# Kernel tuning notes

Hardware: AMD Instinct MI355X
Metric: run time of the kernel (lower is better)

Reference implementation:

```python
import jax, jax.numpy as jnp
import numpy as np
import math

NUM_HEADS = 16


def _alibi_slopes(num_heads: int):
    # geometric sequence for power-of-2 head counts (paper's scheme)
    def slopes_pow2(n):
        start = 2.0 ** (-(2.0 ** (-(math.log2(n) - 3))))
        return [start * (start ** i) for i in range(n)]
    if math.log2(num_heads).is_integer():
        return slopes_pow2(num_heads)
    c = 2 ** math.floor(math.log2(num_heads))
    extra = slopes_pow2(2 * c)[0::2][: num_heads - c]
    return slopes_pow2(c) + extra


def setup_inputs() -> dict:
    key = jax.random.key(0)
    kq, kk, kv = jax.random.split(key, 3)
    B, H, S, D = 2, NUM_HEADS, 2048, 64
    q = jax.random.normal(kq, (B, H, S, D), dtype=jnp.float32)
    k = jax.random.normal(kk, (B, H, S, D), dtype=jnp.float32)
    v = jax.random.normal(kv, (B, H, S, D), dtype=jnp.float32)
    return {"q": q, "k": k, "v": v}


def reference(q, k, v):
    B, H, Sq, D = q.shape
    Sk = k.shape[2]
    slopes = jnp.asarray(_alibi_slopes(H), dtype=jnp.float32)  # [H]
    pos = jnp.arange(Sk)
    # abs relative positions (symmetric, non-causal) as in the source
    rel = jnp.abs(pos[None, :] - pos[:, None]).astype(jnp.float32)  # [Sk, Sk]
    alibi = -slopes[:, None, None] * rel[None, :Sq, :]  # [H, Sq, Sk]
    scores = jnp.einsum("bhqd,bhkd->bhqk", q, k) / math.sqrt(D)
    scores = scores + alibi[None]
    probs = jax.nn.softmax(scores, axis=-1)
    return jnp.einsum("bhqk,bhkd->bhqd", probs, v)
```

## Files before the change

kernel.cpp:

```cpp
#include <hip/hip_runtime.h>
#include <hip/hip_bf16.h>
#include <math.h>

typedef __bf16 bf16;
typedef __attribute__((ext_vector_type(8))) bf16 bf16x8;
typedef __attribute__((ext_vector_type(2))) bf16 bf16x2;
typedef __attribute__((ext_vector_type(16))) float f32x16;
typedef __attribute__((ext_vector_type(4))) unsigned int uint4v;

#define SQ 2048
#define DH 64
#define NH 16
#define QBLK 64
#define KVT 64
#define NKVT (SQ / KVT)
#define LOG2E 1.44269504088896340736f

#define PBUF  16384
#define LDSV  8192
#define LDS_BYTES 32768

__device__ __forceinline__ int swz(int row, int colbyte) {
    return row * 128 + (colbyte ^ ((row & 7) << 4));
}

__device__ __forceinline__ float fast_exp2(float x) {
#if __has_builtin(__builtin_amdgcn_exp2f)
    return __builtin_amdgcn_exp2f(x);
#else
    return exp2f(x);
#endif
}

__device__ __forceinline__ unsigned pkbf16(float a, float b) {
    union { bf16x2 h; unsigned u; } x;
    x.h = (bf16x2){(bf16)a, (bf16)b};
    return x.u;
}

#if __has_builtin(__builtin_amdgcn_permlane32_swap)
__device__ __forceinline__ void plswap(unsigned &a, unsigned &b) {
    typedef __attribute__((ext_vector_type(2))) unsigned int uint2v;
    uint2v r = __builtin_amdgcn_permlane32_swap(a, b, false, false);
    a = r[0]; b = r[1];
}
#else
__device__ __forceinline__ void plswap(unsigned &a, unsigned &b) {
    asm volatile("v_permlane32_swap_b32 %0, %1" : "+v"(a), "+v"(b));
}
#endif

#if __has_builtin(__builtin_amdgcn_global_load_lds)
#define HAVE_GLL 1
__device__ __forceinline__ void async_copy16(const bf16* g, char* l) {
    __builtin_amdgcn_global_load_lds(
        (const __attribute__((address_space(1))) unsigned int*)g,
        (__attribute__((address_space(3))) unsigned int*)l, 16, 0, 0);
}
#else
#define HAVE_GLL 0
#endif

union FragU { uint4v u; bf16x8 b; };

__global__ __launch_bounds__(256)
void alibi_prep_kernel(const float* __restrict__ K, const float* __restrict__ V,
                       bf16* __restrict__ Kb, bf16* __restrict__ Vtb) {
    __shared__ bf16 lt[64][72];
    const int t  = threadIdx.x;
    const int s0 = blockIdx.x * 64;
    const int bh = blockIdx.y;
    if (blockIdx.z == 0) {
        const float* src = K + (size_t)bh * SQ * DH + (size_t)s0 * DH;
        bf16* dst = Kb + (size_t)bh * SQ * DH + (size_t)s0 * DH;
#pragma unroll
        for (int i = 0; i < 2; ++i) {
            int idx = t + 256 * i;
            int row = idx >> 3, c8 = idx & 7;
            const float* p = src + row * DH + c8 * 8;
            float4 a = *(const float4*)p, b = *(const float4*)(p + 4);
            bf16x8 pk = {(bf16)a.x,(bf16)a.y,(bf16)a.z,(bf16)a.w,
                         (bf16)b.x,(bf16)b.y,(bf16)b.z,(bf16)b.w};
            *(bf16x8*)(dst + row * DH + c8 * 8) = pk;
        }
    } else {
        const float* src = V + (size_t)bh * SQ * DH + (size_t)s0 * DH;
#pragma unroll
        for (int i = 0; i < 2; ++i) {
            int idx = t + 256 * i;
            int row = idx >> 3, c8 = idx & 7;
            const float* p = src + row * DH + c8 * 8;
            float4 a = *(const float4*)p, b = *(const float4*)(p + 4);
            bf16 e[8] = {(bf16)a.x,(bf16)a.y,(bf16)a.z,(bf16)a.w,
                         (bf16)b.x,(bf16)b.y,(bf16)b.z,(bf16)b.w};
#pragma unroll
            for (int j = 0; j < 8; ++j) lt[c8 * 8 + j][row] = e[j];
        }
        __syncthreads();
        bf16* dst = Vtb + (size_t)bh * DH * SQ;
#pragma unroll
        for (int i = 0; i < 2; ++i) {
            int idx = t + 256 * i;
            int d = idx >> 3, c8 = idx & 7;
            *(bf16x8*)(dst + (size_t)d * SQ + s0 + c8 * 8) = *(const bf16x8*)&lt[d][c8 * 8];
        }
    }
}

__global__ __launch_bounds__(256, 4)
void alibi_attn_kernel(const float* __restrict__ Q, const bf16* __restrict__ Kb,
                       const bf16* __restrict__ Vtb, float* __restrict__ Out) {
    __shared__ __align__(16) char lds[LDS_BYTES];
    const int tid   = threadIdx.x;
    const int lane  = tid & 63;
    const int wave  = tid >> 6;
    const int par   = wave >> 1;
    const int kind  = wave & 1;
    const int qhalf = wave & 1;
    const int r32   = lane & 31;
    const int hi    = lane >> 5;
    const int l8    = lane >> 3;

    const int b  = blockIdx.x;
    const int qd = b >> 8, i = b & 255;
    int r;
    if      (qd == 0) r = i;
    else if (qd == 1) r = 511 - i;
    else if (qd == 2) r = 512 + i;
    else              r = 1023 - i;
    const int h   = 15 - (r >> 6);
    const int sub = r & 63;
    const int bh  = (sub >> 5) * NH + h;
    const int q0  = (sub & 31) * QBLK;

    const float slope2  = exp2f(-0.5f * (float)(h + 1)) * LOG2E;
    const float SLOPE2N = -slope2;
    const float QSCALE  = 0.125f * LOG2E;

    const int D = (int)(24.0f / slope2);
    const int a0 = q0 - D;
    const int tmin = (a0 <= 0) ? 0 : (a0 >> 6);
    const int tmax = min(NKVT - 1, (q0 + QBLK - 1 + D) >> 6);
    const int nsteps = ((tmax - tmin + 1) + 1) >> 1;

    const size_t base = (size_t)bh * SQ * DH;
    const float* Qp = Q + base;
    const bf16*  Kp = Kb + base;
    const bf16*  Vp = Vtb + base;
    float*       Op = Out + base;

    const int qrow = q0 + qhalf * 32 + r32;
    bf16x8 qfrag[4];
#pragma unroll
    for (int dstep = 0; dstep < 4; ++dstep) {
        const float* sq = Qp + (size_t)qrow * DH + dstep * 16 + hi * 8;
        float4 a = *(const float4*)sq, bb = *(const float4*)(sq + 4);
        qfrag[dstep] = (bf16x8){(bf16)(a.x*QSCALE),(bf16)(a.y*QSCALE),
                                (bf16)(a.z*QSCALE),(bf16)(a.w*QSCALE),
                                (bf16)(bb.x*QSCALE),(bf16)(bb.y*QSCALE),
                                (bf16)(bb.z*QSCALE),(bf16)(bb.w*QSCALE)};
    }

    f32x16 oacc[2];
#pragma unroll
    for (int d = 0; d < 2; ++d)
#pragma unroll
        for (int rr = 0; rr < 16; ++rr) oacc[d][rr] = 0.f;
    float ps0 = 0.f, ps1 = 0.f, ps2 = 0.f, ps3 = 0.f;
    const float qh = (float)(qrow - 4 * hi);

    const int cswz = ((lane & 7) << 4) ^ (l8 << 4);
    char* const sbuf = lds + par * PBUF + kind * LDSV;
    const char* const cbuf = lds + par * PBUF;

    for (int s = 0; s < nsteps; ++s) {
        const int tc = tmin + 2 * s + par;
        const int ts = min(tc, tmax);

        {
            const int kv0s = ts * KVT;
            if (kind == 0) {
#pragma unroll
                for (int c = 0; c < 8; ++c) {
                    const int row = c * 8 + l8;
                    const bf16* gK = Kp + (size_t)(kv0s + row) * DH + (cswz >> 1);
#if HAVE_GLL
                    async_copy16(gK, sbuf + c * 1024);
#else
                    *(bf16x8*)(sbuf + c * 1024 + lane * 16) = *(const bf16x8*)gK;
#endif
                }
            } else {
#pragma unroll
                for (int c = 0; c < 8; ++c) {
                    const int row = c * 8 + l8;
                    const bf16* gV = Vp + (size_t)row * SQ + kv0s + (cswz >> 1);
#if HAVE_GLL
                    async_copy16(gV, sbuf + c * 1024);
#else
                    *(bf16x8*)(sbuf + c * 1024 + lane * 16) = *(const bf16x8*)gV;
#endif
                }
            }
        }
        asm volatile("s_waitcnt vmcnt(0)" ::: "memory");
        __builtin_amdgcn_s_barrier();
        __builtin_amdgcn_sched_barrier(0);

        if (tc <= tmax) {
            const int kv0 = tc * KVT;

            f32x16 sacc[2];
            __builtin_amdgcn_s_setprio(1);
#pragma unroll
            for (int blk = 0; blk < 2; ++blk) {
                f32x16 acc;
#pragma unroll
                for (int rr = 0; rr < 16; ++rr) acc[rr] = 0.f;
#pragma unroll
                for (int dstep = 0; dstep < 4; ++dstep) {
                    bf16x8 kf = *(const bf16x8*)(cbuf + swz(blk * 32 + r32, dstep * 32 + hi * 16));
                    acc = __builtin_amdgcn_mfma_f32_32x32x16_bf16(kf, qfrag[dstep], acc, 0, 0, 0);
                }
                sacc[blk] = acc;
            }
            __builtin_amdgcn_s_setprio(0);

            const float gq = qh - (float)kv0;
            float p[32];
#pragma unroll
            for (int blk = 0; blk < 2; ++blk)
#pragma unroll
                for (int reg = 0; reg < 16; ++reg) {
                    const int krel = (reg & 3) + 8 * (reg >> 2) + 32 * blk;
                    float d = gq - (float)krel;
                    float s2 = fmaf(SLOPE2N, fabsf(d), sacc[blk][reg]);
                    float e = fast_exp2(s2);
                    p[blk * 16 + reg] = e;
                    if ((reg & 3) == 0) ps0 += e;
                    else if ((reg & 3) == 1) ps1 += e;
                    else if ((reg & 3) == 2) ps2 += e;
                    else ps3 += e;
                }

            __builtin_amdgcn_s_setprio(1);
#pragma unroll
            for (int kstep = 0; kstep < 4; ++kstep) {
                const int b16 = (kstep >> 1) * 16;
                const int R = (kstep & 1) * 8;
                unsigned w0 = pkbf16(p[b16 + R + 0], p[b16 + R + 1]);
                unsigned w1 = pkbf16(p[b16 + R + 2], p[b16 + R + 3]);
                unsigned w2 = pkbf16(p[b16 + R + 4], p[b16 + R + 5]);
                unsigned w3 = pkbf16(p[b16 + R + 6], p[b16 + R + 7]);
                plswap(w0, w2);
                plswap(w1, w3);
                FragU pf; pf.u = (uint4v){w0, w1, w2, w3};
#pragma unroll
                for (int dblk = 0; dblk < 2; ++dblk) {
                    bf16x8 vf = *(const bf16x8*)(cbuf + LDSV + swz(dblk * 32 + r32, kstep * 32 + hi * 16));
                    oacc[dblk] = __builtin_amdgcn_mfma_f32_32x32x16_bf16(vf, pf.b, oacc[dblk], 0, 0, 0);
                }
            }
            __builtin_amdgcn_s_setprio(0);
        }
        __builtin_amdgcn_s_barrier();
        __builtin_amdgcn_sched_barrier(0);
    }

    float psum = (ps0 + ps1) + (ps2 + ps3);
    psum += __shfl_xor(psum, 32);

    __syncthreads();
    float* ep = (float*)lds + qhalf * (64 * 36);
    float* slot = ep + lane * 36;
    if (par == 1) {
#pragma unroll
        for (int dblk = 0; dblk < 2; ++dblk)
#pragma unroll
            for (int g2 = 0; g2 < 4; ++g2)
                *(float4*)(slot + dblk * 16 + g2 * 4) =
                    (float4){oacc[dblk][4*g2+0], oacc[dblk][4*g2+1],
                             oacc[dblk][4*g2+2], oacc[dblk][4*g2+3]};
        slot[32] = psum;
    }
    __syncthreads();
    if (par == 0) {
#pragma unroll
        for (int dblk = 0; dblk < 2; ++dblk)
#pragma unroll
            for (int g2 = 0; g2 < 4; ++g2) {
                float4 o = *(const float4*)(slot + dblk * 16 + g2 * 4);
                oacc[dblk][4*g2+0] += o.x; oacc[dblk][4*g2+1] += o.y;
                oacc[dblk][4*g2+2] += o.z; oacc[dblk][4*g2+3] += o.w;
            }
        psum += slot[32];

        const float inv = 1.f / psum;
#pragma unroll
        for (int dblk = 0; dblk < 2; ++dblk)
#pragma unroll
            for (int g2 = 0; g2 < 4; ++g2) {
                float4 o = {oacc[dblk][4*g2+0] * inv, oacc[dblk][4*g2+1] * inv,
                            oacc[dblk][4*g2+2] * inv, oacc[dblk][4*g2+3] * inv};
                *(float4*)(Op + (size_t)qrow * DH + dblk * 32 + g2 * 8 + hi * 4) = o;
            }
    }
}

extern "C" void kernel_launch(void* const* d_in, const int* in_sizes, int n_in,
                              void* d_out, int out_size, void* d_ws, size_t ws_size,
                              hipStream_t stream) {
    const float* q = (const float*)d_in[0];
    const float* k = (const float*)d_in[1];
    const float* v = (const float*)d_in[2];
    float* out = (float*)d_out;
    const int BH = in_sizes[0] / (SQ * DH);
    bf16* Kb  = (bf16*)d_ws;
    bf16* Vtb = (bf16*)((char*)d_ws + (size_t)BH * SQ * DH * sizeof(bf16));
    alibi_prep_kernel<<<dim3(SQ / 64, BH, 2), dim3(256), 0, stream>>>(k, v, Kb, Vtb);
    const int nblk = BH * (SQ / QBLK);
    alibi_attn_kernel<<<dim3(nblk), dim3(256), 0, stream>>>(q, Kb, Vtb, out);
}
```

Baseline: 49.67 us.

## Load K/V fragments directly from global memory into registers, dropping LDS staging

Removes the cooperative async global-to-LDS staging of K and V tiles and the per-step barriers. Each wave now loads its own K and V MFMA fragments straight from global memory into registers, with the V loads issued before the softmax so their latency overlaps it. This removes barrier synchronisation between waves, at the cost of duplicate global/L2 traffic because both q-half waves fetch the same K/V tiles. It also raises register pressure from holding 16 fragments at once. The early __syncthreads before the epilogue is dropped because the exchange buffer is no longer shared with the tile staging.

New measurement: 90.93 us. 83.1% more time.

```diff
diff --git a/kernel.cpp b/kernel.cpp
--- a/kernel.cpp
+++ b/kernel.cpp
@@ -16,14 +16,6 @@
 #define NKVT (SQ / KVT)
 #define LOG2E 1.44269504088896340736f
 
-#define PBUF  16384
-#define LDSV  8192
-#define LDS_BYTES 32768
-
-__device__ __forceinline__ int swz(int row, int colbyte) {
-    return row * 128 + (colbyte ^ ((row & 7) << 4));
-}
-
 __device__ __forceinline__ float fast_exp2(float x) {
 #if __has_builtin(__builtin_amdgcn_exp2f)
     return __builtin_amdgcn_exp2f(x);
@@ -48,17 +40,6 @@
 __device__ __forceinline__ void plswap(unsigned &a, unsigned &b) {
     asm volatile("v_permlane32_swap_b32 %0, %1" : "+v"(a), "+v"(b));
 }
-#endif
-
-#if __has_builtin(__builtin_amdgcn_global_load_lds)
-#define HAVE_GLL 1
-__device__ __forceinline__ void async_copy16(const bf16* g, char* l) {
-    __builtin_amdgcn_global_load_lds(
-        (const __attribute__((address_space(1))) unsigned int*)g,
-        (__attribute__((address_space(3))) unsigned int*)l, 16, 0, 0);
-}
-#else
-#define HAVE_GLL 0
 #endif
 
 union FragU { uint4v u; bf16x8 b; };
@@ -110,16 +91,14 @@
 __global__ __launch_bounds__(256, 4)
 void alibi_attn_kernel(const float* __restrict__ Q, const bf16* __restrict__ Kb,
                        const bf16* __restrict__ Vtb, float* __restrict__ Out) {
-    __shared__ __align__(16) char lds[LDS_BYTES];
+    __shared__ float ex[2][64][36];
     const int tid   = threadIdx.x;
     const int lane  = tid & 63;
     const int wave  = tid >> 6;
     const int par   = wave >> 1;
-    const int kind  = wave & 1;
     const int qhalf = wave & 1;
     const int r32   = lane & 31;
     const int hi    = lane >> 5;
-    const int l8    = lane >> 3;
 
     const int b  = blockIdx.x;
     const int qd = b >> 8, i = b & 255;
@@ -141,7 +120,6 @@
     const int a0 = q0 - D;
     const int tmin = (a0 <= 0) ? 0 : (a0 >> 6);
     const int tmax = min(NKVT - 1, (q0 + QBLK - 1 + D) >> 6);
-    const int nsteps = ((tmax - tmin + 1) + 1) >> 1;
 
     const size_t base = (size_t)bh * SQ * DH;
     const float* Qp = Q + base;
@@ -169,110 +147,79 @@
     float ps0 = 0.f, ps1 = 0.f, ps2 = 0.f, ps3 = 0.f;
     const float qh = (float)(qrow - 4 * hi);
 
-    const int cswz = ((lane & 7) << 4) ^ (l8 << 4);
-    char* const sbuf = lds + par * PBUF + kind * LDSV;
-    const char* const cbuf = lds + par * PBUF;
-
-    for (int s = 0; s < nsteps; ++s) {
-        const int tc = tmin + 2 * s + par;
-        const int ts = min(tc, tmax);
-
-        {
-            const int kv0s = ts * KVT;
-            if (kind == 0) {
-#pragma unroll
-                for (int c = 0; c < 8; ++c) {
-                    const int row = c * 8 + l8;
-                    const bf16* gK = Kp + (size_t)(kv0s + row) * DH + (cswz >> 1);
-#if HAVE_GLL
-                    async_copy16(gK, sbuf + c * 1024);
-#else
-                    *(bf16x8*)(sbuf + c * 1024 + lane * 16) = *(const bf16x8*)gK;
-#endif
-                }
-            } else {
-#pragma unroll
-                for (int c = 0; c < 8; ++c) {
-                    const int row = c * 8 + l8;
-                    const bf16* gV = Vp + (size_t)row * SQ + kv0s + (cswz >> 1);
-#if HAVE_GLL
-                    async_copy16(gV, sbuf + c * 1024);
-#else
-                    *(bf16x8*)(sbuf + c * 1024 + lane * 16) = *(const bf16x8*)gV;
-#endif
-                }
+    for (int tc = tmin + par; tc <= tmax; tc += 2) {
+        const int kv0 = tc * KVT;
+
+        bf16x8 kf[8];
+#pragma unroll
+        for (int blk = 0; blk < 2; ++blk)
+#pragma unroll
+            for (int dstep = 0; dstep < 4; ++dstep)
+                kf[blk * 4 + dstep] =
+                    *(const bf16x8*)(Kp + (size_t)(kv0 + blk * 32 + r32) * DH + dstep * 16 + hi * 8);
+
+        f32x16 sacc[2];
+        __builtin_amdgcn_s_setprio(1);
+#pragma unroll
+        for (int blk = 0; blk < 2; ++blk) {
+            f32x16 acc;
+#pragma unroll
+            for (int rr = 0; rr < 16; ++rr) acc[rr] = 0.f;
+#pragma unroll
+            for (int dstep = 0; dstep < 4; ++dstep)
+                acc = __builtin_amdgcn_mfma_f32_32x32x16_bf16(kf[blk * 4 + dstep], qfrag[dstep], acc, 0, 0, 0);
+            sacc[blk] = acc;
+        }
+        __builtin_amdgcn_s_setprio(0);
+
+        bf16x8 vf[8];
+#pragma unroll
+        for (int kstep = 0; kstep < 4; ++kstep)
+#pragma unroll
+            for (int dblk = 0; dblk < 2; ++dblk)
+                vf[kstep * 2 + dblk] =
+                    *(const bf16x8*)(Vp + (size_t)(dblk * 32 + r32) * SQ + kv0 + kstep * 16 + hi * 8);
+
+        const float gq = qh - (float)kv0;
+        float p[32];
+#pragma unroll
+        for (int blk = 0; blk < 2; ++blk)
+#pragma unroll
+            for (int reg = 0; reg < 16; ++reg) {
+                const int krel = (reg & 3) + 8 * (reg >> 2) + 32 * blk;
+                float d = gq - (float)krel;
+                float s2 = fmaf(SLOPE2N, fabsf(d), sacc[blk][reg]);
+                float e = fast_exp2(s2);
+                p[blk * 16 + reg] = e;
+                if ((reg & 3) == 0) ps0 += e;
+                else if ((reg & 3) == 1) ps1 += e;
+                else if ((reg & 3) == 2) ps2 += e;
+                else ps3 += e;
             }
-        }
-        asm volatile("s_waitcnt vmcnt(0)" ::: "memory");
-        __builtin_amdgcn_s_barrier();
-        __builtin_amdgcn_sched_barrier(0);
-
-        if (tc <= tmax) {
-            const int kv0 = tc * KVT;
-
-            f32x16 sacc[2];
-            __builtin_amdgcn_s_setprio(1);
-#pragma unroll
-            for (int blk = 0; blk < 2; ++blk) {
-                f32x16 acc;
-#pragma unroll
-                for (int rr = 0; rr < 16; ++rr) acc[rr] = 0.f;
-#pragma unroll
-                for (int dstep = 0; dstep < 4; ++dstep) {
-                    bf16x8 kf = *(const bf16x8*)(cbuf + swz(blk * 32 + r32, dstep * 32 + hi * 16));
-                    acc = __builtin_amdgcn_mfma_f32_32x32x16_bf16(kf, qfrag[dstep], acc, 0, 0, 0);
-                }
-                sacc[blk] = acc;
-            }
-            __builtin_amdgcn_s_setprio(0);
-
-            const float gq = qh - (float)kv0;
-            float p[32];
-#pragma unroll
-            for (int blk = 0; blk < 2; ++blk)
-#pragma unroll
-                for (int reg = 0; reg < 16; ++reg) {
-                    const int krel = (reg & 3) + 8 * (reg >> 2) + 32 * blk;
-                    float d = gq - (float)krel;
-                    float s2 = fmaf(SLOPE2N, fabsf(d), sacc[blk][reg]);
-                    float e = fast_exp2(s2);
-                    p[blk * 16 + reg] = e;
-                    if ((reg & 3) == 0) ps0 += e;
-                    else if ((reg & 3) == 1) ps1 += e;
-                    else if ((reg & 3) == 2) ps2 += e;
-                    else ps3 += e;
-                }
-
-            __builtin_amdgcn_s_setprio(1);
-#pragma unroll
-            for (int kstep = 0; kstep < 4; ++kstep) {
-                const int b16 = (kstep >> 1) * 16;
-                const int R = (kstep & 1) * 8;
-                unsigned w0 = pkbf16(p[b16 + R + 0], p[b16 + R + 1]);
-                unsigned w1 = pkbf16(p[b16 + R + 2], p[b16 + R + 3]);
-                unsigned w2 = pkbf16(p[b16 + R + 4], p[b16 + R + 5]);
-                unsigned w3 = pkbf16(p[b16 + R + 6], p[b16 + R + 7]);
-                plswap(w0, w2);
-                plswap(w1, w3);
-                FragU pf; pf.u = (uint4v){w0, w1, w2, w3};
-#pragma unroll
-                for (int dblk = 0; dblk < 2; ++dblk) {
-                    bf16x8 vf = *(const bf16x8*)(cbuf + LDSV + swz(dblk * 32 + r32, kstep * 32 + hi * 16));
-                    oacc[dblk] = __builtin_amdgcn_mfma_f32_32x32x16_bf16(vf, pf.b, oacc[dblk], 0, 0, 0);
-                }
-            }
-            __builtin_amdgcn_s_setprio(0);
-        }
-        __builtin_amdgcn_s_barrier();
-        __builtin_amdgcn_sched_barrier(0);
+
+        __builtin_amdgcn_s_setprio(1);
+#pragma unroll
+        for (int kstep = 0; kstep < 4; ++kstep) {
+            const int b16 = (kstep >> 1) * 16;
+            const int R = (kstep & 1) * 8;
+            unsigned w0 = pkbf16(p[b16 + R + 0], p[b16 + R + 1]);
+            unsigned w1 = pkbf16(p[b16 + R + 2], p[b16 + R + 3]);
+            unsigned w2 = pkbf16(p[b16 + R + 4], p[b16 + R + 5]);
+            unsigned w3 = pkbf16(p[b16 + R + 6], p[b16 + R + 7]);
+            plswap(w0, w2);
+            plswap(w1, w3);
+            FragU pf; pf.u = (uint4v){w0, w1, w2, w3};
+#pragma unroll
+            for (int dblk = 0; dblk < 2; ++dblk)
+                oacc[dblk] = __builtin_amdgcn_mfma_f32_32x32x16_bf16(vf[kstep * 2 + dblk], pf.b, oacc[dblk], 0, 0, 0);
+        }
+        __builtin_amdgcn_s_setprio(0);
     }
 
     float psum = (ps0 + ps1) + (ps2 + ps3);
     psum += __shfl_xor(psum, 32);
 
-    __syncthreads();
-    float* ep = (float*)lds + qhalf * (64 * 36);
-    float* slot = ep + lane * 36;
+    float* slot = &ex[qhalf][lane][0];
     if (par == 1) {
 #pragma unroll
         for (int dblk = 0; dblk < 2; ++dblk)
```
